# Kernel tuning notes

Hardware: AMD Instinct MI355X
Metric: run time of the kernel (lower is better)

Reference implementation:

```python
import jax, jax.numpy as jnp
import numpy as np

N = 50000
E = 800000
IN_C, HID, OUT_C, DEPTH, HEADS = 3, 128, 64, 4, 4
EPS = 1e-6
NEG_SLOPE = 0.2  # PyG GATConv default leaky_relu slope


def setup_inputs() -> dict:
    key = jax.random.key(0)
    ks = jax.random.split(key, 12)
    x = jax.random.normal(ks[0], (N, IN_C), dtype=jnp.float32)
    edge_index = jax.random.randint(ks[1], (2, E), 0, N, dtype=jnp.int32)
    s = 0.05
    return {
        "x": x,
        "edge_index": edge_index,
        "W_in": jax.random.normal(ks[2], (IN_C, HID), dtype=jnp.float32) * s,
        "b_in": jnp.zeros((HID,), jnp.float32),
        # per-layer GATConv params, stacked over depth
        "W_conv": jax.random.normal(ks[3], (DEPTH, HID, HEADS * HID), dtype=jnp.float32) * s,
        "att_src": jax.random.normal(ks[4], (DEPTH, HEADS, HID), dtype=jnp.float32) * s,
        "att_dst": jax.random.normal(ks[5], (DEPTH, HEADS, HID), dtype=jnp.float32) * s,
        "b_conv": jnp.zeros((DEPTH, HID), jnp.float32),
        "ln_gamma": jnp.ones((DEPTH, HID), jnp.float32),
        "ln_beta": jnp.zeros((DEPTH, HID), jnp.float32),
        "W_out": jax.random.normal(ks[6], (HID, OUT_C), dtype=jnp.float32) * s,
        "b_out": jnp.zeros((OUT_C,), jnp.float32),
    }


def _layer_norm(x, gamma, beta):
    mu = jnp.mean(x, axis=-1, keepdims=True)
    var = jnp.mean(jnp.square(x - mu), axis=-1, keepdims=True)
    return (x - mu) * jax.lax.rsqrt(var + EPS) * gamma + beta


def _gat_conv(x, src, dst, W, a_src, a_dst, bias):
    # x: [N, HID]; src/dst: [E2] (self-loops already appended)
    xh = (x @ W).reshape(N, HEADS, HID)                       # [N, H, C]
    alpha_s = jnp.einsum("nhc,hc->nh", xh, a_src)             # [N, H]
    alpha_d = jnp.einsum("nhc,hc->nh", xh, a_dst)             # [N, H]
    e = jax.nn.leaky_relu(alpha_s[src] + alpha_d[dst], NEG_SLOPE)  # [E2, H]
    # segment softmax over incoming edges of each destination node
    m = jax.ops.segment_max(e, dst, num_segments=N)           # [N, H]
    p = jnp.exp(e - m[dst])                                   # [E2, H]
    z = jax.ops.segment_sum(p, dst, num_segments=N)           # [N, H]
    alpha = p / z[dst]                                        # [E2, H]
    msg = alpha[:, :, None] * xh[src]                         # [E2, H, C]
    out = jax.ops.segment_sum(msg, dst, num_segments=N)       # [N, H, C]
    # concat=False -> mean over heads, then bias
    return out.mean(axis=1) + bias


def reference(x, edge_index, W_in, b_in, W_conv, att_src, att_dst, b_conv,
              ln_gamma, ln_beta, W_out, b_out):
    # add self-loops (PyG GATConv default add_self_loops=True)
    loops = jnp.arange(N, dtype=edge_index.dtype)
    src = jnp.concatenate([edge_index[0], loops])
    dst = jnp.concatenate([edge_index[1], loops])

    h = x @ W_in + b_in
    for i in range(DEPTH):
        residual = h
        h = _layer_norm(h, ln_gamma[i], ln_beta[i])
        h = _gat_conv(h, src, dst, W_conv[i], att_src[i], att_dst[i], b_conv[i])
        h = jax.nn.relu(h)
        h = h + residual
    return h @ W_out + b_out
```

## Files before the change

kernel.cpp:

```cpp
#include <hip/hip_runtime.h>
#include <hip/hip_fp16.h>
#include <math.h>

#define N_NODES 50000
#define E_EDGES 800000
#define E2 (E_EDGES + N_NODES)
#define HID 128
#define HEADS 4
#define OUTC 64
#define DEPTH 4
#define NEG_SLOPE 0.2f
#define LN_EPS 1e-6f
#define NT2 3125

typedef float f32x4 __attribute__((ext_vector_type(4)));
typedef float f32x2 __attribute__((ext_vector_type(2)));
typedef _Float16 half8 __attribute__((ext_vector_type(8)));


__global__ void k_deg(const int* __restrict__ ei, int* __restrict__ deg) {
    int e = blockIdx.x * 256 + threadIdx.x;
    if (e >= E2) return;
    int d = (e < E_EDGES) ? ei[E_EDGES + e] : (e - E_EDGES);
    atomicAdd(&deg[d], 1);
}

__global__ void k_scan_block(const int* __restrict__ deg, int* __restrict__ partial,
                             int* __restrict__ bsum, int n) {
    __shared__ int sm[1024];
    int i = blockIdx.x * 1024 + threadIdx.x;
    int v = (i < n) ? deg[i] : 0;
    sm[threadIdx.x] = v;
    __syncthreads();
    for (int off = 1; off < 1024; off <<= 1) {
        int t = (threadIdx.x >= off) ? sm[threadIdx.x - off] : 0;
        __syncthreads();
        sm[threadIdx.x] += t;
        __syncthreads();
    }
    if (i < n) partial[i] = sm[threadIdx.x];
    if (threadIdx.x == 1023) bsum[blockIdx.x] = sm[1023];
}

__global__ void k_scan_bsum(int* __restrict__ bsum, int nb) {
    if (threadIdx.x == 0 && blockIdx.x == 0) {
        int run = 0;
        for (int b = 0; b < nb; ++b) { int v = bsum[b]; bsum[b] = run; run += v; }
    }
}

__global__ void k_scan_fix(const int* __restrict__ deg, int* __restrict__ row_ptr,
                           const int* __restrict__ bsum, int n) {
    int i = blockIdx.x * 1024 + threadIdx.x;
    if (i < n) row_ptr[i] = row_ptr[i] - deg[i] + bsum[blockIdx.x];
    if (i == 0) row_ptr[n] = E2;
}

__global__ void k_fill(const int* __restrict__ ei, const int* __restrict__ row_ptr,
                       int* __restrict__ cur, int* __restrict__ csr_src) {
    int e = blockIdx.x * 256 + threadIdx.x;
    if (e >= E2) return;
    int s, d;
    if (e < E_EDGES) { s = ei[e]; d = ei[E_EDGES + e]; } else { s = d = e - E_EDGES; }
    int pos = atomicAdd(&cur[d], 1);
    csr_src[row_ptr[d] + pos] = s;
}


__global__ void k_ws(const float* __restrict__ W_conv, const float* __restrict__ att_s,
                     const float* __restrict__ att_d, float* __restrict__ ws_all) {
    int idx = blockIdx.x * 256 + threadIdx.x;
    if (idx >= DEPTH * 1024) return;
    int j = idx & 7, c = (idx >> 3) & 127, layer = idx >> 10;
    int hh = j & 3, sd = j >> 2;
    const float* Wr = W_conv + (size_t)layer * 65536 + (size_t)c * 512 + hh * HID;
    const float* at = (sd ? att_d : att_s) + (size_t)layer * HEADS * HID + hh * HID;
    float s = 0.f;
    for (int cc = 0; cc < HID; ++cc) s += Wr[cc] * at[cc];
    ws_all[idx] = s;
}


__global__ void k_repackB2(const float* __restrict__ W_conv, _Float16* __restrict__ Bp) {
    int idx = blockIdx.x * 256 + threadIdx.x;
    if (idx >= DEPTH * 65536) return;
    int jj    = idx & 7;
    int lane  = (idx >> 3) & 63;
    int kc    = (idx >> 9) & 15;
    int ntile = (idx >> 13) & 7;
    int layer = idx >> 16;
    int k = kc * 32 + (lane >> 4) * 8 + jj;
    int n = ntile * 16 + (lane & 15);
    int hh = k >> 7;
    int s  = k & 127;
    int c  = (s & 7) * 16 + (s >> 3);
    Bp[idx] = (_Float16)(0.25f * W_conv[(size_t)layer * 65536 + (size_t)c * 512 + hh * HID + n]);
}


__global__ void k_repackBout(const float* __restrict__ W_out, _Float16* __restrict__ Bout) {
    int idx = blockIdx.x * 256 + threadIdx.x;
    if (idx >= 8192) return;
    int j    = idx & 7;
    int lane = (idx >> 3) & 63;
    int nt   = (idx >> 9) & 3;
    int kc   = idx >> 11;
    int k = kc * 32 + (lane >> 4) * 8 + j;
    int c = (k & 7) * 16 + (k >> 3);
    int n = nt * 16 + (lane & 15);
    Bout[idx] = (_Float16)W_out[(size_t)c * OUTC + n];
}


__global__ __launch_bounds__(256) void k_in_proj_ln(const float* __restrict__ x,
                                                    const float* __restrict__ W,
                                                    const float* __restrict__ bias,
                                                    const float* __restrict__ gamma,
                                                    const float* __restrict__ beta,
                                                    const float* __restrict__ ws,
                                                    float* __restrict__ h,
                                                    unsigned char* __restrict__ ln8,
                                                    float* __restrict__ as_,
                                                    float* __restrict__ ad_) {
    int tid = threadIdx.x;
    int lane = tid & 63;
    int nd = blockIdx.x * 4 + (tid >> 6);
    const float* xr = x + nd * 3;
    float x0 = xr[0], x1 = xr[1], x2 = xr[2];
    int j0 = lane, j1 = lane + 64;
    float a = bias[j0] + x0 * W[j0] + x1 * W[HID + j0] + x2 * W[2 * HID + j0];
    float b = bias[j1] + x0 * W[j1] + x1 * W[HID + j1] + x2 * W[2 * HID + j1];
    size_t base = (size_t)nd * HID;
    h[base + j0] = a;
    h[base + j1] = b;
    float s = a + b;
    for (int o = 1; o < 64; o <<= 1) s += __shfl_xor(s, o);
    float mu = s * (1.0f / 128.0f);
    float da = a - mu, db = b - mu;
    float v = da * da + db * db;
    for (int o = 1; o < 64; o <<= 1) v += __shfl_xor(v, o);
    float rstd = rsqrtf(v * (1.0f / 128.0f) + LN_EPS);
    float va = da * rstd * gamma[j0] + beta[j0];
    float vb = db * rstd * gamma[j1] + beta[j1];

    float ap[8];
    for (int j = 0; j < 8; ++j)
        ap[j] = va * ws[j0 * 8 + j] + vb * ws[j1 * 8 + j];
    for (int o = 1; o < 64; o <<= 1)
        for (int j = 0; j < 8; ++j) ap[j] += __shfl_xor(ap[j], o);
    if (lane == 0) {
        for (int hh = 0; hh < 4; ++hh) {
            as_[nd * 4 + hh] = ap[hh];
            ad_[nd * 4 + hh] = ap[4 + hh];
        }
    }

    float pv[8];
    for (int t = 0; t < 8; ++t) {
        int c = t * 16 + (lane & 15);
        float s1 = __shfl(va, c & 63);
        float s2 = __shfl(vb, c & 63);
        pv[t] = (c < 64) ? s1 : s2;
    }
    if (lane < 16) {
        int w0 = __builtin_amdgcn_cvt_pk_fp8_f32(pv[0], pv[1], 0, false);
        w0     = __builtin_amdgcn_cvt_pk_fp8_f32(pv[2], pv[3], w0, true);
        int w1 = __builtin_amdgcn_cvt_pk_fp8_f32(pv[4], pv[5], 0, false);
        w1     = __builtin_amdgcn_cvt_pk_fp8_f32(pv[6], pv[7], w1, true);
        *(int2*)(ln8 + base + lane * 8) = make_int2(w0, w1);
    }
}


__global__ __launch_bounds__(256) void k_layer(const unsigned char* __restrict__ ln8r,
                                               const int* __restrict__ row_ptr,
                                               const int* __restrict__ csr_src,
                                               const float* __restrict__ asr,
                                               const float* __restrict__ adr,
                                               const _Float16* __restrict__ Bp,
                                               const float* __restrict__ ws,
                                               const float* __restrict__ bias,
                                               const float* __restrict__ gamma,
                                               const float* __restrict__ beta,
                                               float* __restrict__ h,
                                               unsigned char* __restrict__ ln8w,
                                               float* __restrict__ asw,
                                               float* __restrict__ adw,
                                               _Float16* __restrict__ h16,
                                               int write_ln, int last) {
    __shared__ _Float16 Afr[8192];
    __shared__ float Cts[16][132];
    int tid  = threadIdx.x;
    int lane = tid & 63;
    int w    = tid >> 6;
    int g    = lane >> 4;
    int l    = lane & 15;
    int quad = lane >> 4;
    int l15  = lane & 15;
    int tile = blockIdx.x;
    int m    = w * 4 + g;
    int nd   = tile * 16 + m;

    int e0 = row_ptr[nd], e1 = row_ptr[nd + 1];
    float4 ad4 = *(const float4*)(adr + (size_t)nd * 4);

    f32x2 a00 = (f32x2)(0.f), a01 = (f32x2)(0.f), a02 = (f32x2)(0.f), a03 = (f32x2)(0.f);
    f32x2 a10 = (f32x2)(0.f), a11 = (f32x2)(0.f), a12 = (f32x2)(0.f), a13 = (f32x2)(0.f);
    f32x2 a20 = (f32x2)(0.f), a21 = (f32x2)(0.f), a22 = (f32x2)(0.f), a23 = (f32x2)(0.f);
    f32x2 a30 = (f32x2)(0.f), a31 = (f32x2)(0.f), a32 = (f32x2)(0.f), a33 = (f32x2)(0.f);
    float4 zz = make_float4(0.f, 0.f, 0.f, 0.f);

    const unsigned char* xb = ln8r + l * 8;

#define EDGE_P(Q, P) do {                                                   \
    float t_;                                                               \
    t_ = (Q).x + ad4.x; t_ = (t_ >= 0.f) ? t_ : NEG_SLOPE * t_; (P).x = __expf(t_); \
    t_ = (Q).y + ad4.y; t_ = (t_ >= 0.f) ? t_ : NEG_SLOPE * t_; (P).y = __expf(t_); \
    t_ = (Q).z + ad4.z; t_ = (t_ >= 0.f) ? t_ : NEG_SLOPE * t_; (P).z = __expf(t_); \
    t_ = (Q).w + ad4.w; t_ = (t_ >= 0.f) ? t_ : NEG_SLOPE * t_; (P).w = __expf(t_); \
} while (0)

#define ACC_EDGE(P, X) do {                                                 \
    f32x2 v0 = __builtin_amdgcn_cvt_pk_f32_fp8((X).x, false);               \
    f32x2 v1 = __builtin_amdgcn_cvt_pk_f32_fp8((X).x, true);                \
    f32x2 v2 = __builtin_amdgcn_cvt_pk_f32_fp8((X).y, false);               \
    f32x2 v3 = __builtin_amdgcn_cvt_pk_f32_fp8((X).y, true);                \
    a00 += (f32x2)((P).x) * v0; a01 += (f32x2)((P).x) * v1;                 \
    a02 += (f32x2)((P).x) * v2; a03 += (f32x2)((P).x) * v3;                 \
    a10 += (f32x2)((P).y) * v0; a11 += (f32x2)((P).y) * v1;                 \
    a12 += (f32x2)((P).y) * v2; a13 += (f32x2)((P).y) * v3;                 \
    a20 += (f32x2)((P).z) * v0; a21 += (f32x2)((P).z) * v1;                 \
    a22 += (f32x2)((P).z) * v2; a23 += (f32x2)((P).z) * v3;                 \
    a30 += (f32x2)((P).w) * v0; a31 += (f32x2)((P).w) * v1;                 \
    a32 += (f32x2)((P).w) * v2; a33 += (f32x2)((P).w) * v3;                 \
    zz.x += (P).x; zz.y += (P).y; zz.z += (P).z; zz.w += (P).w;             \
} while (0)

    int e = e0;
    for (; e + 2 <= e1; e += 2) {
        int s0 = csr_src[e];
        int s1 = csr_src[e + 1];
        float4 q0 = *(const float4*)(asr + (size_t)s0 * 4);
        float4 q1 = *(const float4*)(asr + (size_t)s1 * 4);
        int2 x0 = *(const int2*)(xb + (size_t)s0 * 128);
        int2 x1 = *(const int2*)(xb + (size_t)s1 * 128);
        float4 p0, p1;
        EDGE_P(q0, p0);
        EDGE_P(q1, p1);
        ACC_EDGE(p0, x0);
        ACC_EDGE(p1, x1);
    }
    if (e < e1) {
        int s0 = csr_src[e];
        float4 q0 = *(const float4*)(asr + (size_t)s0 * 4);
        int2 x0 = *(const int2*)(xb + (size_t)s0 * 128);
        float4 p0;
        EDGE_P(q0, p0);
        ACC_EDGE(p0, x0);
    }
#undef EDGE_P
#undef ACC_EDGE

    {
        f32x2 i0 = (f32x2)(1.0f / zz.x), i1 = (f32x2)(1.0f / zz.y);
        f32x2 i2 = (f32x2)(1.0f / zz.z), i3 = (f32x2)(1.0f / zz.w);
        a00 *= i0; a01 *= i0; a02 *= i0; a03 *= i0;
        a10 *= i1; a11 *= i1; a12 *= i1; a13 *= i1;
        a20 *= i2; a21 *= i2; a22 *= i2; a23 *= i2;
        a30 *= i3; a31 *= i3; a32 *= i3; a33 *= i3;
        int fl = (l & 3) * 16 + m;
        int kb = l >> 2;
        union { _Float16 hx[8]; int4 v4; } cf;
#define STORE_HEAD(H, P0, P1, P2, P3) do {                                  \
        cf.hx[0] = (_Float16)P0[0]; cf.hx[1] = (_Float16)P0[1];             \
        cf.hx[2] = (_Float16)P1[0]; cf.hx[3] = (_Float16)P1[1];             \
        cf.hx[4] = (_Float16)P2[0]; cf.hx[5] = (_Float16)P2[1];             \
        cf.hx[6] = (_Float16)P3[0]; cf.hx[7] = (_Float16)P3[1];             \
        *(int4*)(Afr + ((((H) * 4 + kb) * 64 + fl) * 8)) = cf.v4;           \
} while (0)
        STORE_HEAD(0, a00, a01, a02, a03);
        STORE_HEAD(1, a10, a11, a12, a13);
        STORE_HEAD(2, a20, a21, a22, a23);
        STORE_HEAD(3, a30, a31, a32, a33);
#undef STORE_HEAD
    }
    __syncthreads();

    {
        int nt0 = w * 2, nt1 = w * 2 + 1;
        f32x4 c0 = (f32x4)(0.f), c1 = (f32x4)(0.f);
        const _Float16* b0p = Bp + (size_t)nt0 * 8192 + lane * 8;
        const _Float16* b1p = Bp + (size_t)nt1 * 8192 + lane * 8;
        #pragma unroll
        for (int kc = 0; kc < 16; ++kc) {
            half8 a  = *(const half8*)(Afr + (kc * 64 + lane) * 8);
            half8 b0 = *(const half8*)(b0p + kc * 512);
            half8 b1 = *(const half8*)(b1p + kc * 512);
            c0 = __builtin_amdgcn_mfma_f32_16x16x32_f16(a, b0, c0, 0, 0, 0);
            c1 = __builtin_amdgcn_mfma_f32_16x16x32_f16(a, b1, c1, 0, 0, 0);
        }
        #pragma unroll
        for (int r = 0; r < 4; ++r) {
            Cts[quad * 4 + r][nt0 * 16 + l15] = c0[r];
            Cts[quad * 4 + r][nt1 * 16 + l15] = c1[r];
        }
    }
    __syncthreads();

    int row = quad * 4 + w;
    int node = tile * 16 + row;
    float* hr = h + (size_t)node * HID;

    float rv[8];
    #pragma unroll
    for (int nt = 0; nt < 8; ++nt) {
        float t = Cts[row][nt * 16 + l15] + bias[nt * 16 + l15];
        t = fmaxf(t, 0.f);
        rv[nt] = t + hr[nt * 16 + l15];
    }
    if (!last) {
        #pragma unroll
        for (int nt = 0; nt < 8; ++nt) hr[nt * 16 + l15] = rv[nt];
    } else {
        union { _Float16 hx[8]; int4 v4; } cf;
        #pragma unroll
        for (int nt = 0; nt < 8; ++nt) cf.hx[nt] = (_Float16)rv[nt];
        int kc = l15 >> 2;
        int lf = (l15 & 3) * 16 + row;
        *(int4*)(h16 + (((size_t)tile * 4 + kc) * 64 + lf) * 8) = cf.v4;
    }

    if (write_ln) {
        float ga[8], be[8], wsv[8][8];
        #pragma unroll
        for (int nt = 0; nt < 8; ++nt) {
            int c = nt * 16 + l15;
            ga[nt] = gamma[c];
            be[nt] = beta[c];
            for (int j = 0; j < 8; ++j) wsv[nt][j] = ws[c * 8 + j];
        }
        float s = 0.f;
        #pragma unroll
        for (int nt = 0; nt < 8; ++nt) s += rv[nt];
        s += __shfl_xor(s, 1); s += __shfl_xor(s, 2);
        s += __shfl_xor(s, 4); s += __shfl_xor(s, 8);
        float mu = s * (1.0f / 128.0f);
        float var = 0.f;
        #pragma unroll
        for (int nt = 0; nt < 8; ++nt) { float d = rv[nt] - mu; var += d * d; }
        var += __shfl_xor(var, 1); var += __shfl_xor(var, 2);
        var += __shfl_xor(var, 4); var += __shfl_xor(var, 8);
        float rstd = rsqrtf(var * (1.0f / 128.0f) + LN_EPS);
        float lnv[8];
        #pragma unroll
        for (int nt = 0; nt < 8; ++nt)
            lnv[nt] = (rv[nt] - mu) * rstd * ga[nt] + be[nt];

        float ap[8];
        #pragma unroll
        for (int j = 0; j < 8; ++j) {
            float t = 0.f;
            for (int nt = 0; nt < 8; ++nt) t += lnv[nt] * wsv[nt][j];
            ap[j] = t;
        }
        #pragma unroll
        for (int j = 0; j < 8; ++j) {
            ap[j] += __shfl_xor(ap[j], 1); ap[j] += __shfl_xor(ap[j], 2);
            ap[j] += __shfl_xor(ap[j], 4); ap[j] += __shfl_xor(ap[j], 8);
        }
        if (l15 == 0) {
            for (int hh = 0; hh < 4; ++hh) {
                asw[node * 4 + hh] = ap[hh];
                adw[node * 4 + hh] = ap[4 + hh];
            }
        }

        int w0 = __builtin_amdgcn_cvt_pk_fp8_f32(lnv[0], lnv[1], 0, false);
        w0     = __builtin_amdgcn_cvt_pk_fp8_f32(lnv[2], lnv[3], w0, true);
        int w1 = __builtin_amdgcn_cvt_pk_fp8_f32(lnv[4], lnv[5], 0, false);
        w1     = __builtin_amdgcn_cvt_pk_fp8_f32(lnv[6], lnv[7], w1, true);
        *(int2*)(ln8w + (size_t)node * 128 + l15 * 8) = make_int2(w0, w1);
    }
}


__global__ __launch_bounds__(256) void k_out_proj_mfma(const _Float16* __restrict__ h16,
                                                       const _Float16* __restrict__ Bout,
                                                       const float* __restrict__ b,
                                                       float* __restrict__ out) {
    int tid = threadIdx.x;
    int lane = tid & 63;
    int tile = blockIdx.x * 4 + (tid >> 6);
    if (tile >= NT2) return;

    const _Float16* ab = h16 + (size_t)tile * 2048 + lane * 8;
    f32x4 acc[4];
    for (int nt = 0; nt < 4; ++nt) acc[nt] = (f32x4)(0.0f);
    #pragma unroll
    for (int kc = 0; kc < 4; ++kc) {
        half8 a = *(const half8*)(ab + kc * 512);
        #pragma unroll
        for (int nt = 0; nt < 4; ++nt) {
            half8 bf = *(const half8*)(Bout + ((size_t)(kc * 4 + nt) * 64 + lane) * 8);
            acc[nt] = __builtin_amdgcn_mfma_f32_16x16x32_f16(a, bf, acc[nt], 0, 0, 0);
        }
    }

    int l15 = lane & 15, quad = lane >> 4;
    float bo[4];
    #pragma unroll
    for (int nt = 0; nt < 4; ++nt) bo[nt] = b[nt * 16 + l15];
    #pragma unroll
    for (int r = 0; r < 4; ++r) {
        int node = tile * 16 + quad * 4 + r;
        float* orow = out + (size_t)node * OUTC;
        #pragma unroll
        for (int nt = 0; nt < 4; ++nt)
            orow[nt * 16 + l15] = acc[nt][r] + bo[nt];
    }
}


extern "C" void kernel_launch(void* const* d_in, const int* in_sizes, int n_in,
                              void* d_out, int out_size, void* d_ws, size_t ws_size,
                              hipStream_t stream) {
    const float* x       = (const float*)d_in[0];
    const int*   ei      = (const int*)d_in[1];
    const float* W_in    = (const float*)d_in[2];
    const float* b_in    = (const float*)d_in[3];
    const float* W_conv  = (const float*)d_in[4];
    const float* att_src = (const float*)d_in[5];
    const float* att_dst = (const float*)d_in[6];
    const float* b_conv  = (const float*)d_in[7];
    const float* ln_g    = (const float*)d_in[8];
    const float* ln_b    = (const float*)d_in[9];
    const float* W_out   = (const float*)d_in[10];
    const float* b_out   = (const float*)d_in[11];
    float* out = (float*)d_out;

    char* ws = (char*)d_ws;
    size_t off = 0;
    auto alloc = [&](size_t bytes) { void* p = ws + off; off = (off + bytes + 255) & ~(size_t)255; return p; };
    float* h            = (float*)alloc((size_t)N_NODES * HID * 4);
    unsigned char* ln8a = (unsigned char*)alloc((size_t)N_NODES * 128);
    unsigned char* ln8b = (unsigned char*)alloc((size_t)N_NODES * 128);
    float* asa          = (float*)alloc((size_t)N_NODES * 4 * 4);
    float* asb          = (float*)alloc((size_t)N_NODES * 4 * 4);
    float* ada          = (float*)alloc((size_t)N_NODES * 4 * 4);
    float* adb          = (float*)alloc((size_t)N_NODES * 4 * 4);
    _Float16* Bp2       = (_Float16*)alloc((size_t)DEPTH * 65536 * 2);
    float* ws_all       = (float*)alloc((size_t)DEPTH * 1024 * 4);
    _Float16* h16       = (_Float16*)alloc((size_t)NT2 * 2048 * 2);
    _Float16* Bout      = (_Float16*)alloc((size_t)8192 * 2);
    int* deg    = (int*)alloc((size_t)N_NODES * 4);
    int* cur    = (int*)alloc((size_t)N_NODES * 4);
    int* row_ptr= (int*)alloc((size_t)(N_NODES + 1) * 4);
    int* csr    = (int*)alloc((size_t)E2 * 4);
    int* bsum   = (int*)alloc(256 * 4);
    (void)ws_size; (void)n_in; (void)in_sizes; (void)out_size;

    hipMemsetAsync(deg, 0, (size_t)N_NODES * 4, stream);
    hipMemsetAsync(cur, 0, (size_t)N_NODES * 4, stream);

    k_deg<<<(E2 + 255) / 256, 256, 0, stream>>>(ei, deg);
    int nb = (N_NODES + 1023) / 1024;
    k_scan_block<<<nb, 1024, 0, stream>>>(deg, row_ptr, bsum, N_NODES);
    k_scan_bsum<<<1, 64, 0, stream>>>(bsum, nb);
    k_scan_fix<<<nb, 1024, 0, stream>>>(deg, row_ptr, bsum, N_NODES);
    k_fill<<<(E2 + 255) / 256, 256, 0, stream>>>(ei, row_ptr, cur, csr);

    k_ws<<<(DEPTH * 1024 + 255) / 256, 256, 0, stream>>>(W_conv, att_src, att_dst, ws_all);
    k_repackB2<<<(DEPTH * 65536 + 255) / 256, 256, 0, stream>>>(W_conv, Bp2);
    k_repackBout<<<32, 256, 0, stream>>>(W_out, Bout);

    k_in_proj_ln<<<N_NODES / 4, 256, 0, stream>>>(x, W_in, b_in, ln_g, ln_b, ws_all,
                                                  h, ln8a, asa, ada);

    for (int i = 0; i < DEPTH; ++i) {
        const float* bcp = b_conv + (size_t)i * HID;
        int write_ln = (i + 1 < DEPTH) ? 1 : 0;
        int last = (i + 1 == DEPTH) ? 1 : 0;
        int nl = (i + 1 < DEPTH) ? i + 1 : i;
        const float* gp = ln_g + (size_t)nl * HID;
        const float* bp = ln_b + (size_t)nl * HID;
        const float* wsp = ws_all + (size_t)nl * 1024;

        const unsigned char* l8r = (i & 1) ? ln8b : ln8a;
        unsigned char*       l8w = (i & 1) ? ln8a : ln8b;
        const float* asr = (i & 1) ? asb : asa;
        float*       asw = (i & 1) ? asa : asb;
        const float* adr = (i & 1) ? adb : ada;
        float*       adw = (i & 1) ? ada : adb;

        k_layer<<<NT2, 256, 0, stream>>>(l8r, row_ptr, csr, asr, adr,
                                         Bp2 + (size_t)i * 65536, wsp,
                                         bcp, gp, bp, h, l8w, asw, adw,
                                         h16, write_ln, last);
    }

    k_out_proj_mfma<<<(NT2 + 3) / 4, 256, 0, stream>>>(h16, Bout, b_out, out);
}
```

Before: 463.5 us.

## Sort nodes by degree for load balance, alias shared memory, raise occupancy

Builds a counting-sort permutation of nodes by in-degree, so each 16-node tile in k_layer handles nodes with similar edge counts, and the per-node output indices go through the permutation. The A-fragment and C-tile shared buffers now share one padded row-major region with an extra barrier between them, which cuts LDS use. Launch bounds now request 8 blocks per SM. The aim is to reduce wave divergence from uneven degree within a tile and to raise occupancy. The cost is three small setup kernels, an extra indirection and barrier, and scattered row writes to h.

```diff
diff --git a/kernel.cpp b/kernel.cpp
--- a/kernel.cpp
+++ b/kernel.cpp
@@ -12,6 +12,7 @@
 #define NEG_SLOPE 0.2f
 #define LN_EPS 1e-6f
 #define NT2 3125
+#define AROW 520
 
 typedef float f32x4 __attribute__((ext_vector_type(4)));
 typedef float f32x2 __attribute__((ext_vector_type(2)));
@@ -64,6 +65,36 @@
     if (e < E_EDGES) { s = ei[e]; d = ei[E_EDGES + e]; } else { s = d = e - E_EDGES; }
     int pos = atomicAdd(&cur[d], 1);
     csr_src[row_ptr[d] + pos] = s;
+}
+
+
+__global__ void k_hist(const int* __restrict__ deg, int* __restrict__ hist) {
+    int n = blockIdx.x * 256 + threadIdx.x;
+    if (n >= N_NODES) return;
+    atomicAdd(&hist[min(deg[n], 255)], 1);
+}
+
+__global__ void k_hscan(const int* __restrict__ hist, int* __restrict__ hcur) {
+    __shared__ int sm[256];
+    int t = threadIdx.x;
+    int v = hist[t];
+    sm[t] = v;
+    __syncthreads();
+    for (int off = 1; off < 256; off <<= 1) {
+        int u = (t >= off) ? sm[t - off] : 0;
+        __syncthreads();
+        sm[t] += u;
+        __syncthreads();
+    }
+    hcur[t] = sm[t] - v;
+}
+
+__global__ void k_permfill(const int* __restrict__ deg, int* __restrict__ hcur,
+                           int* __restrict__ perm) {
+    int n = blockIdx.x * 256 + threadIdx.x;
+    if (n >= N_NODES) return;
+    int pos = atomicAdd(&hcur[min(deg[n], 255)], 1);
+    perm[pos] = n;
 }
 
 
@@ -172,9 +203,10 @@
 }
 
 
-__global__ __launch_bounds__(256) void k_layer(const unsigned char* __restrict__ ln8r,
+__global__ __launch_bounds__(256, 8) void k_layer(const unsigned char* __restrict__ ln8r,
                                                const int* __restrict__ row_ptr,
                                                const int* __restrict__ csr_src,
+                                               const int* __restrict__ perm,
                                                const float* __restrict__ asr,
                                                const float* __restrict__ adr,
                                                const _Float16* __restrict__ Bp,
@@ -188,8 +220,10 @@
                                                float* __restrict__ adw,
                                                _Float16* __restrict__ h16,
                                                int write_ln, int last) {
-    __shared__ _Float16 Afr[8192];
-    __shared__ float Cts[16][132];
+    __shared__ __align__(16) unsigned char smraw[16 * AROW * 2];
+    _Float16* Afr = (_Float16*)smraw;
+    float (*Cts)[132] = (float (*)[132])smraw;
+
     int tid  = threadIdx.x;
     int lane = tid & 63;
     int w    = tid >> 6;
@@ -199,7 +233,7 @@
     int l15  = lane & 15;
     int tile = blockIdx.x;
     int m    = w * 4 + g;
-    int nd   = tile * 16 + m;
+    int nd   = perm[tile * 16 + m];
 
     int e0 = row_ptr[nd], e1 = row_ptr[nd + 1];
     float4 ad4 = *(const float4*)(adr + (size_t)nd * 4);
@@ -268,15 +302,14 @@
         a10 *= i1; a11 *= i1; a12 *= i1; a13 *= i1;
         a20 *= i2; a21 *= i2; a22 *= i2; a23 *= i2;
         a30 *= i3; a31 *= i3; a32 *= i3; a33 *= i3;
-        int fl = (l & 3) * 16 + m;
-        int kb = l >> 2;
+        _Float16* rowp = Afr + m * AROW + l15 * 8;
         union { _Float16 hx[8]; int4 v4; } cf;
 #define STORE_HEAD(H, P0, P1, P2, P3) do {                                  \
         cf.hx[0] = (_Float16)P0[0]; cf.hx[1] = (_Float16)P0[1];             \
         cf.hx[2] = (_Float16)P1[0]; cf.hx[3] = (_Float16)P1[1];             \
         cf.hx[4] = (_Float16)P2[0]; cf.hx[5] = (_Float16)P2[1];             \
         cf.hx[6] = (_Float16)P3[0]; cf.hx[7] = (_Float16)P3[1];             \
-        *(int4*)(Afr + ((((H) * 4 + kb) * 64 + fl) * 8)) = cf.v4;           \
+        *(int4*)(rowp + (H) * 128) = cf.v4;                                 \
 } while (0)
         STORE_HEAD(0, a00, a01, a02, a03);
         STORE_HEAD(1, a10, a11, a12, a13);
@@ -286,19 +319,24 @@
     }
     __syncthreads();
 
+    f32x4 c0 = (f32x4)(0.f), c1 = (f32x4)(0.f);
     {
         int nt0 = w * 2, nt1 = w * 2 + 1;
-        f32x4 c0 = (f32x4)(0.f), c1 = (f32x4)(0.f);
         const _Float16* b0p = Bp + (size_t)nt0 * 8192 + lane * 8;
         const _Float16* b1p = Bp + (size_t)nt1 * 8192 + lane * 8;
+        const _Float16* ar = Afr + (lane & 15) * AROW + (lane >> 4) * 8;
         #pragma unroll
         for (int kc = 0; kc < 16; ++kc) {
-            half8 a  = *(const half8*)(Afr + (kc * 64 + lane) * 8);
+            half8 a  = *(const half8*)(ar + kc * 32);
             half8 b0 = *(const half8*)(b0p + kc * 512);
             half8 b1 = *(const half8*)(b1p + kc * 512);
             c0 = __builtin_amdgcn_mfma_f32_16x16x32_f16(a, b0, c0, 0, 0, 0);
             c1 = __builtin_amdgcn_mfma_f32_16x16x32_f16(a, b1, c1, 0, 0, 0);
         }
+    }
+    __syncthreads();
+    {
+        int nt0 = w * 2, nt1 = w * 2 + 1;
         #pragma unroll
         for (int r = 0; r < 4; ++r) {
             Cts[quad * 4 + r][nt0 * 16 + l15] = c0[r];
@@ -308,7 +346,7 @@
     __syncthreads();
 
     int row = quad * 4 + w;
-    int node = tile * 16 + row;
+    int node = perm[tile * 16 + row];
     float* hr = h + (size_t)node * HID;
 
     float rv[8];
@@ -386,6 +424,7 @@
 
 __global__ __launch_bounds__(256) void k_out_proj_mfma(const _Float16* __restrict__ h16,
                                                        const _Float16* __restrict__ Bout,
+                                                       const int* __restrict__ perm,
                                                        const float* __restrict__ b,
                                                        float* __restrict__ out) {
     int tid = threadIdx.x;
@@ -412,7 +451,7 @@
     for (int nt = 0; nt < 4; ++nt) bo[nt] = b[nt * 16 + l15];
     #pragma unroll
     for (int r = 0; r < 4; ++r) {
-        int node = tile * 16 + quad * 4 + r;
+        int node = perm[tile * 16 + quad * 4 + r];
         float* orow = out + (size_t)node * OUTC;
         #pragma unroll
         for (int nt = 0; nt < 4; ++nt)
@@ -456,11 +495,15 @@
     int* cur    = (int*)alloc((size_t)N_NODES * 4);
     int* row_ptr= (int*)alloc((size_t)(N_NODES + 1) * 4);
     int* csr    = (int*)alloc((size_t)E2 * 4);
+    int* perm   = (int*)alloc((size_t)N_NODES * 4);
+    int* hist   = (int*)alloc(256 * 4);
+    int* hcur   = (int*)alloc(256 * 4);
     int* bsum   = (int*)alloc(256 * 4);
     (void)ws_size; (void)n_in; (void)in_sizes; (void)out_size;
 
     hipMemsetAsync(deg, 0, (size_t)N_NODES * 4, stream);
     hipMemsetAsync(cur, 0, (size_t)N_NODES * 4, stream);
+    hipMemsetAsync(hist, 0, 256 * 4, stream);
 
     k_deg<<<(E2 + 255) / 256, 256, 0, stream>>>(ei, deg);
     int nb = (N_NODES + 1023) / 1024;
@@ -468,6 +511,10 @@
     k_scan_bsum<<<1, 64, 0, stream>>>(bsum, nb);
     k_scan_fix<<<nb, 1024, 0, stream>>>(deg, row_ptr, bsum, N_NODES);
     k_fill<<<(E2 + 255) / 256, 256, 0, stream>>>(ei, row_ptr, cur, csr);
+
+    k_hist<<<(N_NODES + 255) / 256, 256, 0, stream>>>(deg, hist);
+    k_hscan<<<1, 256, 0, stream>>>(hist, hcur);
+    k_permfill<<<(N_NODES + 255) / 256, 256, 0, stream>>>(deg, hcur, perm);
 
     k_ws<<<(DEPTH * 1024 + 255) / 256, 256, 0, stream>>>(W_conv, att_src, att_dst, ws_all);
     k_repackB2<<<(DEPTH * 65536 + 255) / 256, 256, 0, stream>>>(W_conv, Bp2);
@@ -492,11 +539,11 @@
         const float* adr = (i & 1) ? adb : ada;
         float*       adw = (i & 1) ? ada : adb;
 
-        k_layer<<<NT2, 256, 0, stream>>>(l8r, row_ptr, csr, asr, adr,
+        k_layer<<<NT2, 256, 0, stream>>>(l8r, row_ptr, csr, perm, asr, adr,
                                          Bp2 + (size_t)i * 65536, wsp,
                                          bcp, gp, bp, h, l8w, asw, adw,
                                          h16, write_ln, last);
     }
 
-    k_out_proj_mfma<<<(NT2 + 3) / 4, 256, 0, stream>>>(h16, Bout, b_out, out);
-}
+    k_out_proj_mfma<<<(NT2 + 3) / 4, 256, 0, stream>>>(h16, Bout, perm, b_out, out);
+}
```

After: 1.183 ms. +155.2%, slower.
